# Performance work log

Measured on AMD Instinct MI355X. Metric: run time of the kernel, lower is better.

Reference implementation:

```python
import jax, jax.numpy as jnp
import numpy as np

D = 1024      # input_dim
H = 4096      # hidden_dim
E = 8         # expert_count
TOP_K = 2
N = 8192      # tokens
LN_EPS = 1e-5


def setup_inputs() -> dict:
    key = jax.random.key(0)
    ks = jax.random.split(key, 10)
    s_d = 1.0 / np.sqrt(D)
    s_h = 1.0 / np.sqrt(H)
    return {
        "x": jax.random.normal(ks[0], (N, D), dtype=jnp.float32),
        "ln_gamma": jnp.ones((D,), jnp.float32),
        "ln_beta": jnp.zeros((D,), jnp.float32),
        "conf_w": jax.random.uniform(ks[1], (D, 1), jnp.float32, -s_d, s_d),
        "conf_b": jnp.zeros((1,), jnp.float32),
        "router_w": jax.random.uniform(ks[2], (D, E), jnp.float32, -s_d, s_d),
        "router_b": jnp.zeros((E,), jnp.float32),
        "w1": jax.random.uniform(ks[3], (E, D, H), jnp.float32, -s_d, s_d),
        "b1": jax.random.uniform(ks[4], (E, H), jnp.float32, -s_d, s_d),
        "w2": jax.random.uniform(ks[5], (E, H, D), jnp.float32, -s_h, s_h),
        "b2": jax.random.uniform(ks[6], (E, D), jnp.float32, -s_h, s_h),
    }


def reference(x, ln_gamma, ln_beta, conf_w, conf_b, router_w, router_b, w1, b1, w2, b2):
    # LayerNorm (torch default eps=1e-5, affine)
    mu = jnp.mean(x, axis=-1, keepdims=True)
    var = jnp.mean(jnp.square(x - mu), axis=-1, keepdims=True)
    x_norm = (x - mu) * jax.lax.rsqrt(var + LN_EPS) * ln_gamma + ln_beta

    # layer-skip confidence head
    confidence = jax.nn.sigmoid(x_norm @ conf_w + conf_b)  # [N,1]

    # router: softmax -> top-k -> renormalize selected weights
    router_probs = jax.nn.softmax(x_norm @ router_w + router_b, axis=-1)  # [N,E]
    vals, indices = jax.lax.top_k(router_probs, TOP_K)                    # [N,K]
    vals = vals / jnp.sum(vals, axis=-1, keepdims=True)

    # scatter top-k weights into dense per-expert combine weights [N,E]
    combine_w = jnp.zeros((x.shape[0], E), x.dtype).at[
        jnp.arange(x.shape[0])[:, None], indices].add(vals)

    # dispatch/combine: loop over small fixed expert count (dense compute,
    # weighted by combine_w, mathematically identical to per-token dispatch)
    combined = jnp.zeros_like(x)
    for e in range(E):
        h = jax.nn.relu(x_norm @ w1[e] + b1[e])      # [N,H]
        combined = combined + combine_w[:, e:e + 1] * (h @ w2[e] + b2[e])

    output = x + combined
    return output, confidence, x
```

## Files before the change

kernel.cpp:

```cpp
#include <hip/hip_runtime.h>
#include <hip/hip_bf16.h>

#define N_TOK 8192
#define DIM   1024
#define HID   4096
#define NEXP  8
#define CSTR  64
#define RTMAX 72
#define HROWS 16896

using bf16x8 = __attribute__((ext_vector_type(8))) short;
using f32x4  = __attribute__((ext_vector_type(4))) float;

__device__ __forceinline__ void gload_lds16(const void* g, void* l) {
  __builtin_amdgcn_global_load_lds(
      (const __attribute__((address_space(1))) unsigned int*)g,
      (__attribute__((address_space(3))) unsigned int*)l, 16, 0, 0);
}

__device__ __forceinline__ float wredsum(float v) {
#pragma unroll
  for (int off = 32; off > 0; off >>= 1) v += __shfl_xor(v, off, 64);
  return v;
}

__device__ __forceinline__ unsigned short f2bf(float f) {
  __hip_bfloat16 h = __float2bfloat16(f);
  return *reinterpret_cast<unsigned short*>(&h);
}
__device__ __forceinline__ float bf2f(unsigned short u) {
  return __uint_as_float((unsigned)u << 16);
}

__global__ __launch_bounds__(256) void prep_kernel(
    const float* __restrict__ x, const float* __restrict__ gamma, const float* __restrict__ beta,
    const float* __restrict__ conf_w, const float* __restrict__ conf_b,
    const float* __restrict__ rw, const float* __restrict__ rb,
    __hip_bfloat16* __restrict__ xn, float* __restrict__ out,
    int* __restrict__ counts, int* __restrict__ lists, float* __restrict__ wts,
    int2* __restrict__ idx) {
  const int t = blockIdx.x * 4 + (threadIdx.x >> 6);
  const int lane = threadIdx.x & 63;
  const float* xr = x + (size_t)t * DIM;

  float4 xv[4];
#pragma unroll
  for (int q = 0; q < 4; q++) xv[q] = *(const float4*)(xr + q * 256 + lane * 4);

  float s = 0.f, s2 = 0.f;
#pragma unroll
  for (int q = 0; q < 4; q++) {
    s  += xv[q].x + xv[q].y + xv[q].z + xv[q].w;
    s2 += xv[q].x * xv[q].x + xv[q].y * xv[q].y + xv[q].z * xv[q].z + xv[q].w * xv[q].w;
  }
  s = wredsum(s); s2 = wredsum(s2);
  const float mu  = s * (1.f / DIM);
  const float inv = rsqrtf(s2 * (1.f / DIM) - mu * mu + 1e-5f);

  float p[9];
#pragma unroll
  for (int e = 0; e < 9; e++) p[e] = 0.f;

#pragma unroll
  for (int q = 0; q < 4; q++) {
    const int d0 = q * 256 + lane * 4;
    const float4 g4 = *(const float4*)(gamma + d0);
    const float4 b4 = *(const float4*)(beta + d0);
    float v0 = (xv[q].x - mu) * inv * g4.x + b4.x;
    float v1 = (xv[q].y - mu) * inv * g4.y + b4.y;
    float v2 = (xv[q].z - mu) * inv * g4.z + b4.z;
    float v3 = (xv[q].w - mu) * inv * g4.w + b4.w;

    ushort4 st; st.x = f2bf(v0); st.y = f2bf(v1); st.z = f2bf(v2); st.w = f2bf(v3);
    *(ushort4*)((unsigned short*)xn + (size_t)t * DIM + d0) = st;
    *(float4*)(out + (size_t)t * DIM + d0) = xv[q];
    *(float4*)(out + (size_t)N_TOK * DIM + N_TOK + (size_t)t * DIM + d0) = xv[q];

    const float vv[4] = {v0, v1, v2, v3};
#pragma unroll
    for (int j = 0; j < 4; j++) {
      const int d = d0 + j;
      const float v = vv[j];
      p[8] += v * conf_w[d];
      const float4 r0 = *(const float4*)(rw + d * 8);
      const float4 r1 = *(const float4*)(rw + d * 8 + 4);
      p[0] += v * r0.x; p[1] += v * r0.y; p[2] += v * r0.z; p[3] += v * r0.w;
      p[4] += v * r1.x; p[5] += v * r1.y; p[6] += v * r1.z; p[7] += v * r1.w;
    }
  }
#pragma unroll
  for (int e = 0; e < 9; e++) p[e] = wredsum(p[e]);

  if (lane == 0) {
    float L[8];
#pragma unroll
    for (int e = 0; e < 8; e++) L[e] = p[e] + rb[e];
    const float cl = p[8] + conf_b[0];
    out[(size_t)N_TOK * DIM + t] = 1.f / (1.f + expf(-cl));

    float mx = L[0];
#pragma unroll
    for (int e = 1; e < 8; e++) mx = fmaxf(mx, L[e]);
    float pe[8];
#pragma unroll
    for (int e = 0; e < 8; e++) pe[e] = expf(L[e] - mx);
    int i0 = 0; float v0 = pe[0];
#pragma unroll
    for (int e = 1; e < 8; e++) if (pe[e] > v0) { v0 = pe[e]; i0 = e; }
    int i1 = -1; float v1 = -1.f;
#pragma unroll
    for (int e = 0; e < 8; e++) if (e != i0 && pe[e] > v1) { v1 = pe[e]; i1 = e; }
    const float wsum = v0 + v1;
    const float w0 = v0 / wsum, w1 = v1 / wsum;
    int p0 = atomicAdd(&counts[i0 * CSTR], 1);
    lists[i0 * N_TOK + p0] = t; wts[i0 * N_TOK + p0] = w0;
    int p1 = atomicAdd(&counts[i1 * CSTR], 1);
    lists[i1 * N_TOK + p1] = t; wts[i1 * N_TOK + p1] = w1;
    idx[t] = make_int2((i0 << 13) | p0, (i1 << 13) | p1);
  }
}

__global__ void bases_kernel(const int* __restrict__ counts, int* __restrict__ bases,
                             int* __restrict__ meta) {
  if (threadIdx.x == 0) {
    int s = 0, r = 0;
#pragma unroll
    for (int e = 0; e < NEXP; e++) {
      bases[e] = s; meta[e] = r;
      const int c = counts[e * CSTR];
      s += c; r += (c + 255) >> 8;
    }
    meta[NEXP] = r;
  }
}

__global__ __launch_bounds__(256) void transpose_cast64(
    const float* __restrict__ src0, __hip_bfloat16* __restrict__ dst0, int R, int C) {
  __shared__ float tile[64][65];
  const size_t msz = (size_t)R * C;
  const float* src = src0 + blockIdx.z * msz;
  __hip_bfloat16* dst = dst0 + blockIdx.z * msz;
  const int c0 = blockIdx.x * 64, r0 = blockIdx.y * 64;
  const int tid = threadIdx.x;
  const int tx = tid & 15, ty = tid >> 4;
#pragma unroll
  for (int k = 0; k < 4; k++) {
    const int row = ty + k * 16;
    const float4 v = *(const float4*)(src + (size_t)(r0 + row) * C + c0 + tx * 4);
    tile[row][tx * 4 + 0] = v.x; tile[row][tx * 4 + 1] = v.y;
    tile[row][tx * 4 + 2] = v.z; tile[row][tx * 4 + 3] = v.w;
  }
  __syncthreads();
#pragma unroll
  for (int k = 0; k < 4; k++) {
    const int orow = ty + k * 16;
    ushort4 st;
    st.x = f2bf(tile[tx * 4 + 0][orow]);
    st.y = f2bf(tile[tx * 4 + 1][orow]);
    st.z = f2bf(tile[tx * 4 + 2][orow]);
    st.w = f2bf(tile[tx * 4 + 3][orow]);
    *(ushort4*)((unsigned short*)dst + (size_t)(c0 + orow) * R + r0 + tx * 4) = st;
  }
}


#define PHASE_BODY(q, BEXTRA)                                                           \
    {                                                                                   \
      bf16x8 af[2][2];                                                                  \
      BEXTRA                                                                            \
      _Pragma("unroll")                                                                 \
      for (int mm = 0; mm < 2; mm++) {                                                  \
        af[mm][0] = *(const bf16x8*)(Ab + ((q) * 2 + mm) * 2048 + c0);                  \
        af[mm][1] = *(const bf16x8*)(Ab + ((q) * 2 + mm) * 2048 + c1);                  \
      }                                                                                 \
      asm volatile("s_waitcnt lgkmcnt(0)" ::: "memory");                                \
      __builtin_amdgcn_sched_barrier(0);                                                \
      __builtin_amdgcn_s_setprio(1);                                                    \
      _Pragma("unroll")                                                                 \
      for (int mm = 0; mm < 2; mm++)                                                    \
        _Pragma("unroll")                                                               \
        for (int n = 0; n < 4; n++) {                                                   \
          acc[(q) * 2 + mm][n] = __builtin_amdgcn_mfma_f32_16x16x32_bf16(af[mm][0], bfr[n][0], acc[(q) * 2 + mm][n], 0, 0, 0); \
          acc[(q) * 2 + mm][n] = __builtin_amdgcn_mfma_f32_16x16x32_bf16(af[mm][1], bfr[n][1], acc[(q) * 2 + mm][n], 0, 0, 0); \
        }                                                                               \
      __builtin_amdgcn_s_setprio(0);                                                    \
    }

#define GEMM_CORE(NT)                                                                   \
  f32x4 acc[8][4] = {};                                                                 \
  stageB(0, 0); stageB(1, 0); stageB(2, 0); stageB(3, 0);                               \
  stageA(0, 0); stageA(1, 0); stageA(2, 0); stageA(3, 0);                               \
  for (int t = 0; t < (NT); ++t) {                                                      \
    const int p = t & 1;                                                                \
    const char* Ab = smem + p * 65536 + rowAb;                                          \
    const char* Bb = smem + p * 65536 + rowBb;                                          \
    const bool st = (t + 1 < (NT));                                                     \
    bf16x8 bfr[4][2];                                                                   \
    if (st) { stageB(0, t + 1); stageB(1, t + 1);                                       \
              asm volatile("s_waitcnt vmcnt(5)" ::: "memory"); }                        \
    else    { asm volatile("s_waitcnt vmcnt(3)" ::: "memory"); }                        \
    __builtin_amdgcn_s_barrier();                                                       \
    PHASE_BODY(0,                                                                       \
      _Pragma("unroll")                                                                 \
      for (int n = 0; n < 4; n++) {                                                     \
        bfr[n][0] = *(const bf16x8*)(Bb + n * 2048 + c0);                               \
        bfr[n][1] = *(const bf16x8*)(Bb + n * 2048 + c1);                               \
      }                                                                                 \
    )                                                                                   \
    if (st) { stageB(2, t + 1); stageB(3, t + 1);                                       \
              asm volatile("s_waitcnt vmcnt(6)" ::: "memory"); }                        \
    else    { asm volatile("s_waitcnt vmcnt(2)" ::: "memory"); }                        \
    __builtin_amdgcn_s_barrier();                                                       \
    PHASE_BODY(1, )                                                                     \
    if (st) { stageA(0, t + 1); stageA(1, t + 1);                                       \
              asm volatile("s_waitcnt vmcnt(7)" ::: "memory"); }                        \
    else    { asm volatile("s_waitcnt vmcnt(1)" ::: "memory"); }                        \
    __builtin_amdgcn_s_barrier();                                                       \
    PHASE_BODY(2, )                                                                     \
    if (st) { stageA(2, t + 1); stageA(3, t + 1);                                       \
              asm volatile("s_waitcnt vmcnt(8)" ::: "memory"); }                        \
    else    { asm volatile("s_waitcnt vmcnt(0)" ::: "memory"); }                        \
    __builtin_amdgcn_s_barrier();                                                       \
    PHASE_BODY(3, )                                                                     \
  }

#define DECODE_BLOCK()                                                        \
  const int lidx = (int)blockIdx.x;                                           \
  const int panel = lidx / RTMAX;                                             \
  const int rtg = lidx - panel * RTMAX;                                       \
  if (rtg >= meta[NEXP]) return;                                              \
  int e = 0;                                                                  \
  _Pragma("unroll")                                                           \
  for (int k = 1; k < NEXP; k++) if (meta[k] <= rtg) e = k;                   \
  const int rt = rtg - meta[e];                                               \
  const int cnt = counts[e * CSTR];                                           \
  const int hbase = bases[e];

__global__ __launch_bounds__(512) void gemm1_kernel(
    const __hip_bfloat16* __restrict__ xn, const __hip_bfloat16* __restrict__ w1t_b,
    const float* __restrict__ b1, const int* __restrict__ lists,
    const int* __restrict__ counts, const int* __restrict__ bases,
    const int* __restrict__ meta, __hip_bfloat16* __restrict__ hbuf) {
  DECODE_BLOCK()
  const int ct = panel;
  const int* list = lists + e * N_TOK;
  const __hip_bfloat16* w1t = w1t_b + (size_t)e * DIM * HID;

  __shared__ char smem[131072];
  const int tid = threadIdx.x;
  const int l = tid & 63;
  const int w = tid >> 6;
  const int wr = w >> 2;
  const int wc = w & 3;

  const int schunk = ((l & 7) ^ ((l >> 3) & 7)) * 8;
  const unsigned short* srcAp[4];
  const unsigned short* srcBp[4];
  int ldsA[4], ldsB[4];
#pragma unroll
  for (int u = 0; u < 4; u++) {
    const int abase = u * 32 + (w >> 2) * 128 + (w & 3) * 8;
    const int arow = abase + (l >> 3);
    const int pos = rt * 256 + arow;
    const int tok = list[pos < cnt ? pos : 0];
    srcAp[u] = (const unsigned short*)xn + (size_t)tok * DIM + schunk;
    ldsA[u] = abase * 128 + l * 16;
    const int bbase = u * 64 + w * 8;
    srcBp[u] = (const unsigned short*)w1t + (size_t)(ct * 256 + bbase + (l >> 3)) * DIM + schunk;
    ldsB[u] = 32768 + bbase * 128 + l * 16;
  }
  auto stageA = [&](int u, int tt) {
    gload_lds16(srcAp[u] + tt * 64, smem + (tt & 1) * 65536 + ldsA[u]);
  };
  auto stageB = [&](int u, int tt) {
    gload_lds16(srcBp[u] + tt * 64, smem + (tt & 1) * 65536 + ldsB[u]);
  };

  const int lr = l & 15;
  const int c0 = (((l >> 4) + 0) ^ (l & 7)) << 4;
  const int c1 = (((l >> 4) + 4) ^ (l & 7)) << 4;
  const int rowAb = (wr * 128 + lr) * 128;
  const int rowBb = 32768 + (wc * 64 + lr) * 128;

  GEMM_CORE(DIM / 64)

  __builtin_amdgcn_s_barrier();
#pragma unroll
  for (int n = 0; n < 4; n++) {
    const int col = wc * 64 + n * 16 + lr;
    const float bv = b1[e * HID + ct * 256 + col];
#pragma unroll
    for (int m = 0; m < 8; m++) {
      f32x4 v = acc[m][n];
#pragma unroll
      for (int j = 0; j < 4; j++) {
        const int row = wr * 128 + m * 16 + (l >> 4) * 4 + j;
        ((unsigned short*)smem)[row * 256 + col] = f2bf(fmaxf(v[j] + bv, 0.f));
      }
    }
  }
  asm volatile("s_waitcnt lgkmcnt(0)" ::: "memory");
  __builtin_amdgcn_s_barrier();
  const int erow0 = tid >> 5, ech = (tid & 31) * 8;
#pragma unroll
  for (int i = 0; i < 16; i++) {
    const int row = i * 16 + erow0;
    const int pos = rt * 256 + row;
    if (pos < cnt) {
      bf16x8 vv = *(const bf16x8*)((const unsigned short*)smem + row * 256 + ech);
      *(bf16x8*)((unsigned short*)hbuf + (size_t)(hbase + pos) * HID + ct * 256 + ech) = vv;
    }
  }
}

__global__ __launch_bounds__(512) void gemm2_kernel(
    const __hip_bfloat16* __restrict__ hbuf, const __hip_bfloat16* __restrict__ w2t_b,
    const int* __restrict__ counts, const int* __restrict__ bases,
    const int* __restrict__ meta, __hip_bfloat16* __restrict__ ybuf, const int SK) {
  DECODE_BLOCK()
  const int ct = panel / SK;
  const int ksp = panel - ct * SK;
  const int kbase = ksp * (HID / SK);
  const __hip_bfloat16* w2t = w2t_b + (size_t)e * DIM * HID;

  __shared__ char smem[131072];
  const int tid = threadIdx.x;
  const int l = tid & 63;
  const int w = tid >> 6;
  const int wr = w >> 2;
  const int wc = w & 3;

  const int schunk = ((l & 7) ^ ((l >> 3) & 7)) * 8;
  const unsigned short* srcAp[4];
  const unsigned short* srcBp[4];
  int ldsA[4], ldsB[4];
#pragma unroll
  for (int u = 0; u < 4; u++) {
    const int abase = u * 32 + (w >> 2) * 128 + (w & 3) * 8;
    const int arow = abase + (l >> 3);
    srcAp[u] = (const unsigned short*)hbuf + (size_t)(hbase + rt * 256 + arow) * HID + kbase + schunk;
    ldsA[u] = abase * 128 + l * 16;
    const int bbase = u * 64 + w * 8;
    srcBp[u] = (const unsigned short*)w2t + (size_t)(ct * 256 + bbase + (l >> 3)) * HID + kbase + schunk;
    ldsB[u] = 32768 + bbase * 128 + l * 16;
  }
  auto stageA = [&](int u, int tt) {
    gload_lds16(srcAp[u] + tt * 64, smem + (tt & 1) * 65536 + ldsA[u]);
  };
  auto stageB = [&](int u, int tt) {
    gload_lds16(srcBp[u] + tt * 64, smem + (tt & 1) * 65536 + ldsB[u]);
  };

  const int lr = l & 15;
  const int c0 = (((l >> 4) + 0) ^ (l & 7)) << 4;
  const int c1 = (((l >> 4) + 4) ^ (l & 7)) << 4;
  const int rowAb = (wr * 128 + lr) * 128;
  const int rowBb = 32768 + (wc * 64 + lr) * 128;

  const int nk = (HID / 64) / SK;
  GEMM_CORE(nk)

  __builtin_amdgcn_s_barrier();
#pragma unroll
  for (int n = 0; n < 4; n++) {
    const int col = wc * 64 + n * 16 + lr;
#pragma unroll
    for (int m = 0; m < 8; m++) {
      f32x4 v = acc[m][n];
#pragma unroll
      for (int j = 0; j < 4; j++) {
        const int row = wr * 128 + m * 16 + (l >> 4) * 4 + j;
        ((unsigned short*)smem)[row * 256 + col] = f2bf(v[j]);
      }
    }
  }
  asm volatile("s_waitcnt lgkmcnt(0)" ::: "memory");
  __builtin_amdgcn_s_barrier();
  const int erow0 = tid >> 5, ech = (tid & 31) * 8;
#pragma unroll
  for (int i = 0; i < 16; i++) {
    const int row = i * 16 + erow0;
    const int pos = rt * 256 + row;
    if (pos < cnt) {
      bf16x8 vv = *(const bf16x8*)((const unsigned short*)smem + row * 256 + ech);
      *(bf16x8*)((unsigned short*)ybuf + ((size_t)ksp * HROWS + hbase + pos) * DIM + ct * 256 + ech) = vv;
    }
  }
}

__global__ __launch_bounds__(256) void combine_kernel(
    const __hip_bfloat16* __restrict__ ybuf, const float* __restrict__ b2,
    const int2* __restrict__ idx, const float* __restrict__ wv,
    const int* __restrict__ bases, float* __restrict__ out, const int SK) {
  const int t = blockIdx.x * 4 + (threadIdx.x >> 6);
  const int lane = threadIdx.x & 63;
  const int2 iv = idx[t];
  const int e0 = iv.x >> 13, p0 = iv.x & (N_TOK - 1);
  const int e1 = iv.y >> 13, p1 = iv.y & (N_TOK - 1);
  const float w0 = wv[iv.x], w1 = wv[iv.y];
  const int r0 = bases[e0] + p0;
  const int r1 = bases[e1] + p1;
#pragma unroll
  for (int q = 0; q < 4; q++) {
    const int d0 = q * 256 + lane * 4;
    float4 o = *(const float4*)(out + (size_t)t * DIM + d0);
    float y0x = 0.f, y0y = 0.f, y0z = 0.f, y0w = 0.f;
    float y1x = 0.f, y1y = 0.f, y1z = 0.f, y1w = 0.f;
    for (int s = 0; s < SK; s++) {
      const ushort4 a = *(const ushort4*)((const unsigned short*)ybuf +
                          ((size_t)s * HROWS + r0) * DIM + d0);
      const ushort4 b = *(const ushort4*)((const unsigned short*)ybuf +
                          ((size_t)s * HROWS + r1) * DIM + d0);
      y0x += bf2f(a.x); y0y += bf2f(a.y); y0z += bf2f(a.z); y0w += bf2f(a.w);
      y1x += bf2f(b.x); y1y += bf2f(b.y); y1z += bf2f(b.z); y1w += bf2f(b.w);
    }
    const float4 bb0 = *(const float4*)(b2 + e0 * DIM + d0);
    const float4 bb1 = *(const float4*)(b2 + e1 * DIM + d0);
    o.x += w0 * (y0x + bb0.x) + w1 * (y1x + bb1.x);
    o.y += w0 * (y0y + bb0.y) + w1 * (y1y + bb1.y);
    o.z += w0 * (y0z + bb0.z) + w1 * (y1z + bb1.z);
    o.w += w0 * (y0w + bb0.w) + w1 * (y1w + bb1.w);
    *(float4*)(out + (size_t)t * DIM + d0) = o;
  }
}

extern "C" void kernel_launch(void* const* d_in, const int* in_sizes, int n_in,
                              void* d_out, int out_size, void* d_ws, size_t ws_size,
                              hipStream_t stream) {
  (void)in_sizes; (void)n_in; (void)out_size;
  const float* x      = (const float*)d_in[0];
  const float* gamma  = (const float*)d_in[1];
  const float* beta   = (const float*)d_in[2];
  const float* conf_w = (const float*)d_in[3];
  const float* conf_b = (const float*)d_in[4];
  const float* rw     = (const float*)d_in[5];
  const float* rb     = (const float*)d_in[6];
  const float* w1     = (const float*)d_in[7];
  const float* b1     = (const float*)d_in[8];
  const float* w2     = (const float*)d_in[9];
  const float* b2     = (const float*)d_in[10];
  float* out = (float*)d_out;

  char* w = (char*)d_ws;
  auto alloc = [&](size_t bytes) { char* p = w; w += (bytes + 255) & ~255ULL; return p; };

  __hip_bfloat16* xn = (__hip_bfloat16*)alloc((size_t)N_TOK * DIM * 2);
  int*   lists  = (int*)alloc((size_t)NEXP * N_TOK * 4);
  float* wtsb   = (float*)alloc((size_t)NEXP * N_TOK * 4);
  int*   counts = (int*)alloc(NEXP * CSTR * 4);
  int*   bases  = (int*)alloc(256);
  int*   meta   = (int*)alloc(256);
  int2*  idx    = (int2*)alloc((size_t)N_TOK * 8);

  const size_t hbufA = (size_t)HROWS * HID * 2;
  const size_t wtA   = (size_t)NEXP * DIM * HID * 2;
  __hip_bfloat16* hbuf = (__hip_bfloat16*)alloc(hbufA);
  __hip_bfloat16* w1t  = (__hip_bfloat16*)alloc(wtA);
  __hip_bfloat16* w2t  = (__hip_bfloat16*)alloc(wtA);
  const size_t used = (size_t)(w - (char*)d_ws);
  const size_t ybuf1 = (size_t)HROWS * DIM * 2;

  int SK;
  __hip_bfloat16* ybuf;
  if (ws_size >= used + 4 * ybuf1 + 4096) {
    SK = 4; ybuf = (__hip_bfloat16*)alloc(4 * ybuf1);
  } else if (ws_size >= used + 2 * ybuf1 + 4096) {
    SK = 2; ybuf = (__hip_bfloat16*)alloc(2 * ybuf1);
  } else {
    SK = 1; ybuf = w1t;
  }

  hipMemsetAsync(counts, 0, NEXP * CSTR * 4, stream);
  prep_kernel<<<N_TOK / 4, 256, 0, stream>>>(x, gamma, beta, conf_w, conf_b, rw, rb,
                                             xn, out, counts, lists, wtsb, idx);
  bases_kernel<<<1, 64, 0, stream>>>(counts, bases, meta);
  transpose_cast64<<<dim3(HID / 64, DIM / 64, NEXP), 256, 0, stream>>>(w1, w1t, DIM, HID);
  transpose_cast64<<<dim3(DIM / 64, HID / 64, NEXP), 256, 0, stream>>>(w2, w2t, HID, DIM);
  gemm1_kernel<<<16 * RTMAX, 512, 0, stream>>>(xn, w1t, b1, lists, counts, bases, meta, hbuf);
  gemm2_kernel<<<4 * SK * RTMAX, 512, 0, stream>>>(hbuf, w2t, counts, bases, meta, ybuf, SK);
  combine_kernel<<<N_TOK / 4, 256, 0, stream>>>(ybuf, b2, idx, wtsb, bases, out, SK);
}
```

Measured before the change: 539.3 us.

## Shrink expert GEMM tiles to 128x256 with K=32 triple-buffered pipeline

Both grouped GEMMs move from 256x256 tiles with K=64 double buffering (128KB LDS) to 128x256 tiles with K=32 and a three-stage LDS ring (72KB). Launch bounds request more resident blocks, and the row-tile granularity in bases_kernel drops to 128. The block index is remapped so panels interleave across eight groups, likely for XCD/L2 locality. This cuts tail padding waste and raises occupancy, at the cost of less operand reuse per tile, more barriers per K step and a two-pass epilogue through LDS.

Result: faster. 510.0 us (-5.4%).

```diff
diff --git a/kernel.cpp b/kernel.cpp
--- a/kernel.cpp
+++ b/kernel.cpp
@@ -6,7 +6,7 @@
 #define HID   4096
 #define NEXP  8
 #define CSTR  64
-#define RTMAX 72
+#define RTMAX 136
 #define HROWS 16896
 
 using bf16x8 = __attribute__((ext_vector_type(8))) short;
@@ -128,7 +128,7 @@
     for (int e = 0; e < NEXP; e++) {
       bases[e] = s; meta[e] = r;
       const int c = counts[e * CSTR];
-      s += c; r += (c + 255) >> 8;
+      s += c; r += (c + 127) >> 7;
     }
     meta[NEXP] = r;
   }
@@ -164,70 +164,47 @@
 }
 
 
-#define PHASE_BODY(q, BEXTRA)                                                           \
-    {                                                                                   \
-      bf16x8 af[2][2];                                                                  \
-      BEXTRA                                                                            \
-      _Pragma("unroll")                                                                 \
-      for (int mm = 0; mm < 2; mm++) {                                                  \
-        af[mm][0] = *(const bf16x8*)(Ab + ((q) * 2 + mm) * 2048 + c0);                  \
-        af[mm][1] = *(const bf16x8*)(Ab + ((q) * 2 + mm) * 2048 + c1);                  \
-      }                                                                                 \
+#define GEMM_CORE(NT)                                                                   \
+  f32x4 acc[4][4] = {};                                                                 \
+  stage(0, 0); stage(1, 24576);                                                         \
+  for (int t = 0; t < (NT); ++t) {                                                      \
+    const int pb = (t % 3) * 24576;                                                     \
+    if (t + 1 < (NT)) { asm volatile("s_waitcnt vmcnt(3)" ::: "memory"); }              \
+    else              { asm volatile("s_waitcnt vmcnt(0)" ::: "memory"); }              \
+    __builtin_amdgcn_s_barrier();                                                       \
+    if (t + 2 < (NT)) stage(t + 2, ((t + 2) % 3) * 24576);                              \
+    const char* Ab = smem + pb + Abase;                                                 \
+    const char* Bb = smem + pb + Bbase;                                                 \
+    bf16x8 bfr[4];                                                                      \
+    _Pragma("unroll")                                                                   \
+    for (int n = 0; n < 4; n++) bfr[n] = *(const bf16x8*)(Bb + n * 1024);               \
+    _Pragma("unroll")                                                                   \
+    for (int qq = 0; qq < 2; qq++) {                                                    \
+      bf16x8 af0 = *(const bf16x8*)(Ab + (qq * 2 + 0) * 1024);                          \
+      bf16x8 af1 = *(const bf16x8*)(Ab + (qq * 2 + 1) * 1024);                          \
       asm volatile("s_waitcnt lgkmcnt(0)" ::: "memory");                                \
       __builtin_amdgcn_sched_barrier(0);                                                \
       __builtin_amdgcn_s_setprio(1);                                                    \
       _Pragma("unroll")                                                                 \
-      for (int mm = 0; mm < 2; mm++)                                                    \
-        _Pragma("unroll")                                                               \
-        for (int n = 0; n < 4; n++) {                                                   \
-          acc[(q) * 2 + mm][n] = __builtin_amdgcn_mfma_f32_16x16x32_bf16(af[mm][0], bfr[n][0], acc[(q) * 2 + mm][n], 0, 0, 0); \
-          acc[(q) * 2 + mm][n] = __builtin_amdgcn_mfma_f32_16x16x32_bf16(af[mm][1], bfr[n][1], acc[(q) * 2 + mm][n], 0, 0, 0); \
-        }                                                                               \
+      for (int n = 0; n < 4; n++) {                                                     \
+        acc[qq * 2 + 0][n] = __builtin_amdgcn_mfma_f32_16x16x32_bf16(af0, bfr[n], acc[qq * 2 + 0][n], 0, 0, 0); \
+        acc[qq * 2 + 1][n] = __builtin_amdgcn_mfma_f32_16x16x32_bf16(af1, bfr[n], acc[qq * 2 + 1][n], 0, 0, 0); \
+      }                                                                                 \
       __builtin_amdgcn_s_setprio(0);                                                    \
-    }
-
-#define GEMM_CORE(NT)                                                                   \
-  f32x4 acc[8][4] = {};                                                                 \
-  stageB(0, 0); stageB(1, 0); stageB(2, 0); stageB(3, 0);                               \
-  stageA(0, 0); stageA(1, 0); stageA(2, 0); stageA(3, 0);                               \
-  for (int t = 0; t < (NT); ++t) {                                                      \
-    const int p = t & 1;                                                                \
-    const char* Ab = smem + p * 65536 + rowAb;                                          \
-    const char* Bb = smem + p * 65536 + rowBb;                                          \
-    const bool st = (t + 1 < (NT));                                                     \
-    bf16x8 bfr[4][2];                                                                   \
-    if (st) { stageB(0, t + 1); stageB(1, t + 1);                                       \
-              asm volatile("s_waitcnt vmcnt(5)" ::: "memory"); }                        \
-    else    { asm volatile("s_waitcnt vmcnt(3)" ::: "memory"); }                        \
-    __builtin_amdgcn_s_barrier();                                                       \
-    PHASE_BODY(0,                                                                       \
-      _Pragma("unroll")                                                                 \
-      for (int n = 0; n < 4; n++) {                                                     \
-        bfr[n][0] = *(const bf16x8*)(Bb + n * 2048 + c0);                               \
-        bfr[n][1] = *(const bf16x8*)(Bb + n * 2048 + c1);                               \
-      }                                                                                 \
-    )                                                                                   \
-    if (st) { stageB(2, t + 1); stageB(3, t + 1);                                       \
-              asm volatile("s_waitcnt vmcnt(6)" ::: "memory"); }                        \
-    else    { asm volatile("s_waitcnt vmcnt(2)" ::: "memory"); }                        \
-    __builtin_amdgcn_s_barrier();                                                       \
-    PHASE_BODY(1, )                                                                     \
-    if (st) { stageA(0, t + 1); stageA(1, t + 1);                                       \
-              asm volatile("s_waitcnt vmcnt(7)" ::: "memory"); }                        \
-    else    { asm volatile("s_waitcnt vmcnt(1)" ::: "memory"); }                        \
-    __builtin_amdgcn_s_barrier();                                                       \
-    PHASE_BODY(2, )                                                                     \
-    if (st) { stageA(2, t + 1); stageA(3, t + 1);                                       \
-              asm volatile("s_waitcnt vmcnt(8)" ::: "memory"); }                        \
-    else    { asm volatile("s_waitcnt vmcnt(0)" ::: "memory"); }                        \
-    __builtin_amdgcn_s_barrier();                                                       \
-    PHASE_BODY(3, )                                                                     \
-  }
-
-#define DECODE_BLOCK()                                                        \
-  const int lidx = (int)blockIdx.x;                                           \
-  const int panel = lidx / RTMAX;                                             \
-  const int rtg = lidx - panel * RTMAX;                                       \
+    }                                                                                   \
+  }
+
+#define DECODE_BLOCK(PPX)                                                     \
+  int panel, rtg;                                                             \
+  if ((PPX) > 0) {                                                            \
+    const int x_ = (int)blockIdx.x & 7;                                       \
+    const int q_ = (int)blockIdx.x >> 3;                                      \
+    rtg = q_ / (PPX);                                                         \
+    panel = x_ * (PPX) + (q_ - rtg * (PPX));                                  \
+  } else {                                                                    \
+    panel = (int)blockIdx.x / RTMAX;                                          \
+    rtg = (int)blockIdx.x - panel * RTMAX;                                    \
+  }                                                                           \
   if (rtg >= meta[NEXP]) return;                                              \
   int e = 0;                                                                  \
   _Pragma("unroll")                                                           \
@@ -236,155 +213,137 @@
   const int cnt = counts[e * CSTR];                                           \
   const int hbase = bases[e];
 
-__global__ __launch_bounds__(512) void gemm1_kernel(
+#define GEMM_COMMON()                                                         \
+  __shared__ char smem[73728];                                                \
+  const int tid = threadIdx.x;                                                \
+  const int l = tid & 63;                                                     \
+  const int w8 = tid >> 6;                                                    \
+  const int wr = w8 >> 2;                                                     \
+  const int wc = w8 & 3;                                                      \
+  const int lr = l & 15;                                                      \
+  const int pchunk = (l >> 4) ^ ((lr >> 1) & 3);                              \
+  const int Abase = (wr * 64 + lr) * 64 + pchunk * 16;                        \
+  const int Bbase = 8192 + (wc * 64 + lr) * 64 + pchunk * 16;                 \
+  const int srow = tid >> 2;                      \
+  const int lc = (tid & 3) ^ ((srow >> 1) & 3);
+
+__global__ __launch_bounds__(512, 4) void gemm1_kernel(
     const __hip_bfloat16* __restrict__ xn, const __hip_bfloat16* __restrict__ w1t_b,
     const float* __restrict__ b1, const int* __restrict__ lists,
     const int* __restrict__ counts, const int* __restrict__ bases,
-    const int* __restrict__ meta, __hip_bfloat16* __restrict__ hbuf) {
-  DECODE_BLOCK()
+    const int* __restrict__ meta, __hip_bfloat16* __restrict__ hbuf, const int ppx) {
+  DECODE_BLOCK(ppx)
   const int ct = panel;
   const int* list = lists + e * N_TOK;
   const __hip_bfloat16* w1t = w1t_b + (size_t)e * DIM * HID;
-
-  __shared__ char smem[131072];
-  const int tid = threadIdx.x;
-  const int l = tid & 63;
-  const int w = tid >> 6;
-  const int wr = w >> 2;
-  const int wc = w & 3;
-
-  const int schunk = ((l & 7) ^ ((l >> 3) & 7)) * 8;
-  const unsigned short* srcAp[4];
-  const unsigned short* srcBp[4];
-  int ldsA[4], ldsB[4];
-#pragma unroll
-  for (int u = 0; u < 4; u++) {
-    const int abase = u * 32 + (w >> 2) * 128 + (w & 3) * 8;
-    const int arow = abase + (l >> 3);
-    const int pos = rt * 256 + arow;
-    const int tok = list[pos < cnt ? pos : 0];
-    srcAp[u] = (const unsigned short*)xn + (size_t)tok * DIM + schunk;
-    ldsA[u] = abase * 128 + l * 16;
-    const int bbase = u * 64 + w * 8;
-    srcBp[u] = (const unsigned short*)w1t + (size_t)(ct * 256 + bbase + (l >> 3)) * DIM + schunk;
-    ldsB[u] = 32768 + bbase * 128 + l * 16;
-  }
-  auto stageA = [&](int u, int tt) {
-    gload_lds16(srcAp[u] + tt * 64, smem + (tt & 1) * 65536 + ldsA[u]);
+  GEMM_COMMON()
+
+  const int apos = rt * 128 + srow;
+  const int tok = list[apos < cnt ? apos : 0];
+  const unsigned short* srcA0 = (const unsigned short*)xn + (size_t)tok * DIM + lc * 8;
+  const unsigned short* srcB0 = (const unsigned short*)w1t + (size_t)(ct * 256 + srow) * DIM + lc * 8;
+  const unsigned short* srcB1 = (const unsigned short*)w1t + (size_t)(ct * 256 + 128 + srow) * DIM + lc * 8;
+
+  auto stage = [&](int tt, int lbase) {
+    gload_lds16(srcA0 + tt * 32, smem + lbase + tid * 16);
+    gload_lds16(srcB0 + tt * 32, smem + lbase + 8192 + tid * 16);
+    gload_lds16(srcB1 + tt * 32, smem + lbase + 16384 + tid * 16);
   };
-  auto stageB = [&](int u, int tt) {
-    gload_lds16(srcBp[u] + tt * 64, smem + (tt & 1) * 65536 + ldsB[u]);
-  };
-
-  const int lr = l & 15;
-  const int c0 = (((l >> 4) + 0) ^ (l & 7)) << 4;
-  const int c1 = (((l >> 4) + 4) ^ (l & 7)) << 4;
-  const int rowAb = (wr * 128 + lr) * 128;
-  const int rowBb = 32768 + (wc * 64 + lr) * 128;
-
-  GEMM_CORE(DIM / 64)
+
+  GEMM_CORE(DIM / 32)
 
   __builtin_amdgcn_s_barrier();
 #pragma unroll
-  for (int n = 0; n < 4; n++) {
-    const int col = wc * 64 + n * 16 + lr;
-    const float bv = b1[e * HID + ct * 256 + col];
-#pragma unroll
-    for (int m = 0; m < 8; m++) {
-      f32x4 v = acc[m][n];
-#pragma unroll
-      for (int j = 0; j < 4; j++) {
-        const int row = wr * 128 + m * 16 + (l >> 4) * 4 + j;
-        ((unsigned short*)smem)[row * 256 + col] = f2bf(fmaxf(v[j] + bv, 0.f));
+  for (int h = 0; h < 2; h++) {
+    if (wr == h) {
+#pragma unroll
+      for (int n = 0; n < 4; n++) {
+        const int col = wc * 64 + n * 16 + lr;
+        const float bv = b1[e * HID + ct * 256 + col];
+#pragma unroll
+        for (int m = 0; m < 4; m++) {
+          f32x4 v = acc[m][n];
+#pragma unroll
+          for (int j = 0; j < 4; j++)
+            ((unsigned short*)smem)[(m * 16 + (l >> 4) * 4 + j) * 256 + col] =
+                f2bf(fmaxf(v[j] + bv, 0.f));
+        }
       }
     }
-  }
-  asm volatile("s_waitcnt lgkmcnt(0)" ::: "memory");
-  __builtin_amdgcn_s_barrier();
-  const int erow0 = tid >> 5, ech = (tid & 31) * 8;
-#pragma unroll
-  for (int i = 0; i < 16; i++) {
-    const int row = i * 16 + erow0;
-    const int pos = rt * 256 + row;
-    if (pos < cnt) {
-      bf16x8 vv = *(const bf16x8*)((const unsigned short*)smem + row * 256 + ech);
-      *(bf16x8*)((unsigned short*)hbuf + (size_t)(hbase + pos) * HID + ct * 256 + ech) = vv;
-    }
-  }
-}
-
-__global__ __launch_bounds__(512) void gemm2_kernel(
+    asm volatile("s_waitcnt lgkmcnt(0)" ::: "memory");
+    __builtin_amdgcn_s_barrier();
+    const int g = tid >> 5, u = tid & 31;
+#pragma unroll
+    for (int i = 0; i < 4; i++) {
+      const int row = i * 16 + g;
+      const int pos = rt * 128 + h * 64 + row;
+      if (pos < cnt) {
+        bf16x8 vv = *(const bf16x8*)((const unsigned short*)smem + row * 256 + u * 8);
+        *(bf16x8*)((unsigned short*)hbuf + (size_t)(hbase + pos) * HID + ct * 256 + u * 8) = vv;
+      }
+    }
+    __builtin_amdgcn_s_barrier();
+  }
+}
+
+__global__ __launch_bounds__(512, 4) void gemm2_kernel(
     const __hip_bfloat16* __restrict__ hbuf, const __hip_bfloat16* __restrict__ w2t_b,
     const int* __restrict__ counts, const int* __restrict__ bases,
-    const int* __restrict__ meta, __hip_bfloat16* __restrict__ ybuf, const int SK) {
-  DECODE_BLOCK()
-  const int ct = panel / SK;
-  const int ksp = panel - ct * SK;
+    const int* __restrict__ meta, __hip_bfloat16* __restrict__ ybuf,
+    const int SK, const int ppx) {
+  DECODE_BLOCK(ppx)
+  const int ct = panel & 3;
+  const int ksp = panel >> 2;
   const int kbase = ksp * (HID / SK);
   const __hip_bfloat16* w2t = w2t_b + (size_t)e * DIM * HID;
-
-  __shared__ char smem[131072];
-  const int tid = threadIdx.x;
-  const int l = tid & 63;
-  const int w = tid >> 6;
-  const int wr = w >> 2;
-  const int wc = w & 3;
-
-  const int schunk = ((l & 7) ^ ((l >> 3) & 7)) * 8;
-  const unsigned short* srcAp[4];
-  const unsigned short* srcBp[4];
-  int ldsA[4], ldsB[4];
-#pragma unroll
-  for (int u = 0; u < 4; u++) {
-    const int abase = u * 32 + (w >> 2) * 128 + (w & 3) * 8;
-    const int arow = abase + (l >> 3);
-    srcAp[u] = (const unsigned short*)hbuf + (size_t)(hbase + rt * 256 + arow) * HID + kbase + schunk;
-    ldsA[u] = abase * 128 + l * 16;
-    const int bbase = u * 64 + w * 8;
-    srcBp[u] = (const unsigned short*)w2t + (size_t)(ct * 256 + bbase + (l >> 3)) * HID + kbase + schunk;
-    ldsB[u] = 32768 + bbase * 128 + l * 16;
-  }
-  auto stageA = [&](int u, int tt) {
-    gload_lds16(srcAp[u] + tt * 64, smem + (tt & 1) * 65536 + ldsA[u]);
+  GEMM_COMMON()
+
+  const unsigned short* srcA0 = (const unsigned short*)hbuf +
+      (size_t)(hbase + rt * 128 + srow) * HID + kbase + lc * 8;
+  const unsigned short* srcB0 = (const unsigned short*)w2t +
+      (size_t)(ct * 256 + srow) * HID + kbase + lc * 8;
+  const unsigned short* srcB1 = (const unsigned short*)w2t +
+      (size_t)(ct * 256 + 128 + srow) * HID + kbase + lc * 8;
+
+  auto stage = [&](int tt, int lbase) {
+    gload_lds16(srcA0 + tt * 32, smem + lbase + tid * 16);
+    gload_lds16(srcB0 + tt * 32, smem + lbase + 8192 + tid * 16);
+    gload_lds16(srcB1 + tt * 32, smem + lbase + 16384 + tid * 16);
   };
-  auto stageB = [&](int u, int tt) {
-    gload_lds16(srcBp[u] + tt * 64, smem + (tt & 1) * 65536 + ldsB[u]);
-  };
-
-  const int lr = l & 15;
-  const int c0 = (((l >> 4) + 0) ^ (l & 7)) << 4;
-  const int c1 = (((l >> 4) + 4) ^ (l & 7)) << 4;
-  const int rowAb = (wr * 128 + lr) * 128;
-  const int rowBb = 32768 + (wc * 64 + lr) * 128;
-
-  const int nk = (HID / 64) / SK;
+
+  const int nk = (HID / 32) / SK;
   GEMM_CORE(nk)
 
   __builtin_amdgcn_s_barrier();
 #pragma unroll
-  for (int n = 0; n < 4; n++) {
-    const int col = wc * 64 + n * 16 + lr;
-#pragma unroll
-    for (int m = 0; m < 8; m++) {
-      f32x4 v = acc[m][n];
-#pragma unroll
-      for (int j = 0; j < 4; j++) {
-        const int row = wr * 128 + m * 16 + (l >> 4) * 4 + j;
-        ((unsigned short*)smem)[row * 256 + col] = f2bf(v[j]);
+  for (int h = 0; h < 2; h++) {
+    if (wr == h) {
+#pragma unroll
+      for (int n = 0; n < 4; n++) {
+        const int col = wc * 64 + n * 16 + lr;
+#pragma unroll
+        for (int m = 0; m < 4; m++) {
+          f32x4 v = acc[m][n];
+#pragma unroll
+          for (int j = 0; j < 4; j++)
+            ((unsigned short*)smem)[(m * 16 + (l >> 4) * 4 + j) * 256 + col] = f2bf(v[j]);
+        }
       }
     }
-  }
-  asm volatile("s_waitcnt lgkmcnt(0)" ::: "memory");
-  __builtin_amdgcn_s_barrier();
-  const int erow0 = tid >> 5, ech = (tid & 31) * 8;
-#pragma unroll
-  for (int i = 0; i < 16; i++) {
-    const int row = i * 16 + erow0;
-    const int pos = rt * 256 + row;
-    if (pos < cnt) {
-      bf16x8 vv = *(const bf16x8*)((const unsigned short*)smem + row * 256 + ech);
-      *(bf16x8*)((unsigned short*)ybuf + ((size_t)ksp * HROWS + hbase + pos) * DIM + ct * 256 + ech) = vv;
-    }
+    asm volatile("s_waitcnt lgkmcnt(0)" ::: "memory");
+    __builtin_amdgcn_s_barrier();
+    const int g = tid >> 5, u = tid & 31;
+#pragma unroll
+    for (int i = 0; i < 4; i++) {
+      const int row = i * 16 + g;
+      const int pos = rt * 128 + h * 64 + row;
+      if (pos < cnt) {
+        bf16x8 vv = *(const bf16x8*)((const unsigned short*)smem + row * 256 + u * 8);
+        *(bf16x8*)((unsigned short*)ybuf +
+                   ((size_t)ksp * HROWS + hbase + pos) * DIM + ct * 256 + u * 8) = vv;
+      }
+    }
+    __builtin_amdgcn_s_barrier();
   }
 }
 
@@ -469,6 +428,9 @@
   } else {
     SK = 1; ybuf = w1t;
   }
+  const int g2panels = 4 * SK;
+  const int g2ppx = (SK == 4) ? 2 : (SK == 2 ? 1 : 0);
+  const int g2grid = g2ppx > 0 ? 8 * g2ppx * RTMAX : g2panels * RTMAX;
 
   hipMemsetAsync(counts, 0, NEXP * CSTR * 4, stream);
   prep_kernel<<<N_TOK / 4, 256, 0, stream>>>(x, gamma, beta, conf_w, conf_b, rw, rb,
@@ -476,7 +438,8 @@
   bases_kernel<<<1, 64, 0, stream>>>(counts, bases, meta);
   transpose_cast64<<<dim3(HID / 64, DIM / 64, NEXP), 256, 0, stream>>>(w1, w1t, DIM, HID);
   transpose_cast64<<<dim3(DIM / 64, HID / 64, NEXP), 256, 0, stream>>>(w2, w2t, HID, DIM);
-  gemm1_kernel<<<16 * RTMAX, 512, 0, stream>>>(xn, w1t, b1, lists, counts, bases, meta, hbuf);
-  gemm2_kernel<<<4 * SK * RTMAX, 512, 0, stream>>>(hbuf, w2t, counts, bases, meta, ybuf, SK);
+  gemm1_kernel<<<8 * 2 * RTMAX, 512, 0, stream>>>(xn, w1t, b1, lists, counts, bases, meta,
+                                                  hbuf, 2);
+  gemm2_kernel<<<g2grid, 512, 0, stream>>>(hbuf, w2t, counts, bases, meta, ybuf, SK, g2ppx);
   combine_kernel<<<N_TOK / 4, 256, 0, stream>>>(ybuf, b2, idx, wtsb, bases, out, SK);
 }
```
